# Kernel optimization log

Hardware: AMD Instinct MI355X
Metric: run time of the kernel (lower is better)

Reference implementation:

```python
import jax, jax.numpy as jnp
import numpy as np

HIDDEN = 2048
NUM_HEADS = 16
HEAD_DIM = HIDDEN // NUM_HEADS  # 128
ROPE_THETA = 10000.0
T = 4096


def _rope(x, positions):
    # x: [T, H, D]; neox-style rotary (rotate halves), matching vLLM get_rope default
    half = HEAD_DIM // 2
    inv_freq = 1.0 / (ROPE_THETA ** (jnp.arange(0, half, dtype=jnp.float32) / half))
    freqs = positions.astype(jnp.float32)[:, None] * inv_freq[None, :]  # [T, half]
    cos = jnp.cos(freqs)[:, None, :]  # [T, 1, half]
    sin = jnp.sin(freqs)[:, None, :]
    x1, x2 = x[..., :half], x[..., half:]
    return jnp.concatenate([x1 * cos - x2 * sin, x2 * cos + x1 * sin], axis=-1)


def setup_inputs() -> dict:
    key = jax.random.key(0)
    k1, k2, k3 = jax.random.split(key, 3)
    return {
        "hidden_states": jax.random.normal(k1, (T, HIDDEN), dtype=jnp.float32),
        "positions": jnp.arange(T, dtype=jnp.int32),
        "w_qkv": jax.random.normal(k2, (HIDDEN, 3 * HIDDEN), dtype=jnp.float32) * (HIDDEN ** -0.5),
        "w_o": jax.random.normal(k3, (HIDDEN, HIDDEN), dtype=jnp.float32) * (HIDDEN ** -0.5),
    }


def reference(hidden_states, positions, w_qkv, w_o):
    qkv = hidden_states @ w_qkv  # [T, 3H]
    q, k, v = jnp.split(qkv, 3, axis=-1)
    q = q.reshape(T, NUM_HEADS, HEAD_DIM)
    k = k.reshape(T, NUM_HEADS, HEAD_DIM)
    v = v.reshape(T, NUM_HEADS, HEAD_DIM)
    q = _rope(q, positions)
    k = _rope(k, positions)
    scale = HEAD_DIM ** -0.5
    # causal SDPA over flattened single sequence
    scores = jnp.einsum("qhd,khd->hqk", q, k) * scale  # [H, T, T]
    causal = jnp.tril(jnp.ones((T, T), dtype=bool))
    scores = jnp.where(causal[None, :, :], scores, jnp.finfo(scores.dtype).min)
    probs = jax.nn.softmax(scores, axis=-1)
    attn = jnp.einsum("hqk,khd->qhd", probs, v).reshape(T, HIDDEN)
    return attn @ w_o
```

## Files before the change

kernel.cpp:

```cpp
#include <hip/hip_runtime.h>
#include <hip/hip_bf16.h>
#include <cstdint>
#include <cstddef>

#define T_SEQ 4096
#define HID   2048
#define NH    16
#define HD    128
#define QKVN  6144
#define KVB   32
#define CHT   16
#define CPH   144

typedef unsigned short u16;
typedef unsigned int u32;
typedef __bf16 bf16x8 __attribute__((ext_vector_type(8)));
typedef __bf16 bf16x4 __attribute__((ext_vector_type(4)));
typedef float  f32x4  __attribute__((ext_vector_type(4)));

typedef const __attribute__((address_space(1))) void* gas_ptr;
typedef __attribute__((address_space(3))) void* las_ptr;

__device__ __forceinline__ void async16(const void* g, void* l) {
  __builtin_amdgcn_global_load_lds((gas_ptr)g, (las_ptr)l, 16, 0, 0);
}

__device__ __forceinline__ u16 f2bf(float f) {
  unsigned int u = __float_as_uint(f);
  u += 0x7fffu + ((u >> 16) & 1u);
  return (u16)(u >> 16);
}

__device__ __forceinline__ float bf2f(u16 x) {
  return __uint_as_float((unsigned)x << 16);
}

__global__ void cast_f32_bf16(const float* __restrict__ in, u16* __restrict__ out, int n) {
  int i = (blockIdx.x * blockDim.x + threadIdx.x) * 4;
  if (i >= n) return;
  float4 v = *(const float4*)&in[i];
  uint2 o;
  o.x = (unsigned)f2bf(v.x) | ((unsigned)f2bf(v.y) << 16);
  o.y = (unsigned)f2bf(v.z) | ((unsigned)f2bf(v.w) << 16);
  *(uint2*)&out[i] = o;
}

__global__ void transpose_cast(const float* __restrict__ in, u16* __restrict__ out,
                               int R, int C) {
  __shared__ float tile[64][65];
  int c0 = blockIdx.x * 64, r0 = blockIdx.y * 64;
  int tid = threadIdx.x;
#pragma unroll
  for (int i = 0; i < 16; ++i) {
    int e = i * 256 + tid;
    int rr = e >> 6, cc = e & 63;
    tile[rr][cc] = in[(size_t)(r0 + rr) * C + c0 + cc];
  }
  __syncthreads();
#pragma unroll
  for (int i = 0; i < 16; ++i) {
    int e = i * 256 + tid;
    int oc = e >> 6, orr = e & 63;
    out[(size_t)(c0 + oc) * R + r0 + orr] = f2bf(tile[orr][oc]);
  }
}

template <typename OUT>
__global__ __launch_bounds__(256)
void gemm_bf16_bt(const u16* __restrict__ A, const u16* __restrict__ BT,
                  OUT* __restrict__ C, int M, int N, int K) {
  __shared__ u16 As[2][128 * 32];
  __shared__ u16 Bs[2][128 * 32];
  int tid = threadIdx.x;
  int row0 = blockIdx.y * 128, col0 = blockIdx.x * 128;
  int wv = tid >> 6, lane = tid & 63, lr = lane & 15, lq = lane >> 4;
  int wm = (wv >> 1) * 64, wn = (wv & 1) * 64;
  f32x4 acc[4][4] = {};

  auto stage = [&](int buf, int ks) {
#pragma unroll
    for (int k = 0; k < 2; ++k) {
      int c = k * 256 + tid;
      int row = c >> 2, col = c & 3;
      int key = (row >> 1) & 3;
      async16(&A[(size_t)(row0 + row) * K + ks + (col ^ key) * 8], &As[buf][c * 8]);
      async16(&BT[(size_t)(col0 + row) * K + ks + (col ^ key) * 8], &Bs[buf][c * 8]);
    }
  };

  stage(0, 0);
  __syncthreads();
  int nk = K >> 5;
  for (int t = 0; t < nk; ++t) {
    int cur = t & 1;
    if (t + 1 < nk) stage(cur ^ 1, (t + 1) * 32);

    const char* AsB = (const char*)&As[cur][0];
    const char* BsB = (const char*)&Bs[cur][0];
    bf16x8 a[4], b[4];
#pragma unroll
    for (int mi = 0; mi < 4; ++mi) {
      int row = wm + mi * 16 + lr;
      a[mi] = *(const bf16x8*)(AsB + row * 64 + ((lq ^ ((row >> 1) & 3)) << 4));
    }
#pragma unroll
    for (int ni = 0; ni < 4; ++ni) {
      int row = wn + ni * 16 + lr;
      b[ni] = *(const bf16x8*)(BsB + row * 64 + ((lq ^ ((row >> 1) & 3)) << 4));
    }
#pragma unroll
    for (int mi = 0; mi < 4; ++mi)
#pragma unroll
      for (int ni = 0; ni < 4; ++ni)
        acc[mi][ni] = __builtin_amdgcn_mfma_f32_16x16x32_bf16(a[mi], b[ni], acc[mi][ni], 0, 0, 0);
    __syncthreads();
  }

#pragma unroll
  for (int mi = 0; mi < 4; ++mi)
#pragma unroll
    for (int ni = 0; ni < 4; ++ni)
#pragma unroll
      for (int r = 0; r < 4; ++r) {
        float v = acc[mi][ni][r];
        size_t idx = (size_t)(row0 + wm + mi * 16 + lq * 4 + r) * N + col0 + wn + ni * 16 + lr;
        if constexpr (sizeof(OUT) == 2) C[idx] = (OUT)f2bf(v);
        else                            C[idx] = (OUT)v;
      }
}

#define SCL2 0.12753224f

__global__ void rope_reorg(const u16* __restrict__ qkv, const int* __restrict__ pos,
                           u16* __restrict__ Qh, u16* __restrict__ Kh) {
  int idx = blockIdx.x * 256 + threadIdx.x;
  if (idx >= T_SEQ * NH * 64) return;
  int d = idx & 63;
  int h = (idx >> 6) & (NH - 1);
  int t = idx >> 10;
  float p = (float)pos[t];
  float inv = exp2f((float)d * -0.20762050594046932f);
  float f = p * inv;
  float s, c;
  __sincosf(f, &s, &c);

  size_t ib = (size_t)t * QKVN + h * HD + d;
  float q1 = bf2f(qkv[ib]), q2 = bf2f(qkv[ib + 64]);
  float k1 = bf2f(qkv[ib + HID]), k2 = bf2f(qkv[ib + HID + 64]);
  size_t ob = ((size_t)h * T_SEQ + t) * HD + d;
  Qh[ob]      = f2bf((q1 * c - q2 * s) * SCL2);
  Qh[ob + 64] = f2bf((q2 * c + q1 * s) * SCL2);
  Kh[ob]      = f2bf(k1 * c - k2 * s);
  Kh[ob + 64] = f2bf(k2 * c + k1 * s);
}

__global__ void vtrans(const u16* __restrict__ qkv, u16* __restrict__ Vt) {
  __shared__ u16 tile[64][136];
  int t0 = blockIdx.x * 64;
  int h = blockIdx.y;
  int tid = threadIdx.x;
#pragma unroll
  for (int i = 0; i < 32; ++i) {
    int e = i * 256 + tid;
    int tt = e >> 7, d = e & 127;
    tile[tt][d] = qkv[(size_t)(t0 + tt) * QKVN + 2 * HID + h * HD + d];
  }
  __syncthreads();
#pragma unroll
  for (int i = 0; i < 32; ++i) {
    int e = i * 256 + tid;
    int d = e >> 6, tt = e & 63;
    Vt[((size_t)h * HD + d) * T_SEQ + t0 + tt] = tile[tt][d];
  }
}

__global__ __launch_bounds__(256)
void attn_fwd(const u16* __restrict__ Qh, const u16* __restrict__ Kh,
              const u16* __restrict__ Vt, u16* __restrict__ Opart,
              float2* __restrict__ ml) {
  __shared__ u16 Ks[2][32 * 128];
  __shared__ u16 Vs[2][128 * 32];
  __shared__ u16 Ps[4][32 * 32];

  int tid = threadIdx.x;
  int wv = tid >> 6, lane = tid & 63, lr = lane & 15, lq = lane >> 4;
  char* PsB = (char*)&Ps[wv][0];

  int id = blockIdx.x;
  int h = id / CPH;
  int w = id - h * CPH;
  int bq = 0, acc = 0;
  for (;;) {
    int ch = (bq + 4) >> 2;
    if (w < acc + ch) break;
    acc += ch;
    ++bq;
  }
  int c = w - acc;
  int nt = 4 * bq + 4;
  int j0 = c * CHT, j1 = min(j0 + CHT, nt);
  int q0 = bq * 128, wrow0 = q0 + wv * 32;

  bf16x8 qf[2][4];
#pragma unroll
  for (int qi = 0; qi < 2; ++qi)
#pragma unroll
    for (int kd = 0; kd < 4; ++kd)
      qf[qi][kd] = *(const bf16x8*)
          &Qh[((size_t)h * T_SEQ + wrow0 + qi * 16 + lr) * HD + kd * 32 + lq * 8];

  f32x4 acc_ot[8][2] = {};
  float m_run[2] = {-1e30f, -1e30f};
  float l_run[2] = {0.0f, 0.0f};

  auto stage = [&](int buf, int jb) {
#pragma unroll
    for (int k = 0; k < 2; ++k) {
      int cc = k * 256 + tid;
      int row = cc >> 4;
      int sc = (cc ^ (row & 7)) & 15;
      async16(&Kh[((size_t)h * T_SEQ + jb + row) * HD + sc * 8], &Ks[buf][cc * 8]);
    }
#pragma unroll
    for (int k = 0; k < 2; ++k) {
      int cc = k * 256 + tid;
      int row = cc >> 2, col = cc & 3;
      int key = (row >> 1) & 3;
      async16(&Vt[((size_t)h * HD + row) * T_SEQ + jb + (col ^ key) * 8],
              &Vs[buf][cc * 8]);
    }
  };

  stage(0, j0 * KVB);
  __syncthreads();

  for (int j = j0; j < j1; ++j) {
    int cur = (j - j0) & 1;
    int jb = j * KVB;
    if (j + 1 < j1) stage(cur ^ 1, jb + KVB);

    if (jb <= wrow0 + 31) {
      const char* KsB = (const char*)&Ks[cur][0];
      const char* VsB = (const char*)&Vs[cur][0];

      f32x4 st[2][2] = {};
#pragma unroll
      for (int kd = 0; kd < 4; ++kd) {
#pragma unroll
        for (int kj = 0; kj < 2; ++kj) {
          int row = kj * 16 + lr;
          int byt = (row << 8) + kd * 64 + lq * 16;
          bf16x8 kf = *(const bf16x8*)(KsB + (byt ^ ((row & 7) << 4)));
#pragma unroll
          for (int qi = 0; qi < 2; ++qi)
            st[kj][qi] = __builtin_amdgcn_mfma_f32_16x16x32_bf16(
                kf, qf[qi][kd], st[kj][qi], 0, 0, 0);
        }
      }

      if (jb + KVB - 1 > wrow0) {
#pragma unroll
        for (int qi = 0; qi < 2; ++qi) {
          int qg = wrow0 + qi * 16 + lr;
#pragma unroll
          for (int kj = 0; kj < 2; ++kj)
#pragma unroll
            for (int r = 0; r < 4; ++r)
              if (jb + kj * 16 + lq * 4 + r > qg) st[kj][qi][r] = -1e30f;
        }
      }

      float sf[2];
#pragma unroll
      for (int qi = 0; qi < 2; ++qi) {
        float mx = fmaxf(fmaxf(fmaxf(st[0][qi][0], st[0][qi][1]),
                               fmaxf(st[0][qi][2], st[0][qi][3])),
                         fmaxf(fmaxf(st[1][qi][0], st[1][qi][1]),
                               fmaxf(st[1][qi][2], st[1][qi][3])));
        mx = fmaxf(mx, __shfl_xor(mx, 16));
        mx = fmaxf(mx, __shfl_xor(mx, 32));
        float mnew = fmaxf(m_run[qi], mx);
        sf[qi] = exp2f(m_run[qi] - mnew);
        m_run[qi] = mnew;

        int rowb = (qi * 16 + lr) * 64;
        int key = ((lr >> 1) & 3) << 4;
        float rs = 0.0f;
#pragma unroll
        for (int kj = 0; kj < 2; ++kj) {
          float p0 = exp2f(st[kj][qi][0] - mnew);
          float p1 = exp2f(st[kj][qi][1] - mnew);
          float p2 = exp2f(st[kj][qi][2] - mnew);
          float p3 = exp2f(st[kj][qi][3] - mnew);
          rs += (p0 + p1) + (p2 + p3);
          bf16x4 pk;
          pk[0] = (__bf16)p0; pk[1] = (__bf16)p1;
          pk[2] = (__bf16)p2; pk[3] = (__bf16)p3;
          *(bf16x4*)(PsB + rowb + (((kj * 16 + lq * 4) * 2) ^ key)) = pk;
        }
        l_run[qi] = l_run[qi] * sf[qi] + rs;
      }

      if (__any((sf[0] < 1.0f) || (sf[1] < 1.0f))) {
#pragma unroll
        for (int di = 0; di < 8; ++di)
#pragma unroll
          for (int qi = 0; qi < 2; ++qi)
#pragma unroll
            for (int r = 0; r < 4; ++r) acc_ot[di][qi][r] *= sf[qi];
      }

      bf16x8 pa[2];
#pragma unroll
      for (int qi = 0; qi < 2; ++qi) {
        int prow = qi * 16 + lr;
        pa[qi] = *(const bf16x8*)(PsB + prow * 64 + ((lq ^ ((lr >> 1) & 3)) << 4));
      }
#pragma unroll
      for (int di = 0; di < 8; ++di) {
        int vrow = di * 16 + lr;
        bf16x8 vb = *(const bf16x8*)(VsB + vrow * 64 + ((lq ^ ((vrow >> 1) & 3)) << 4));
#pragma unroll
        for (int qi = 0; qi < 2; ++qi)
          acc_ot[di][qi] = __builtin_amdgcn_mfma_f32_16x16x32_bf16(
              vb, pa[qi], acc_ot[di][qi], 0, 0, 0);
      }
    }
    __syncthreads();
  }

  u16* Op = Opart + (size_t)id * 128 * 128;
#pragma unroll
  for (int qi = 0; qi < 2; ++qi) {
    float l = l_run[qi];
    l += __shfl_xor(l, 16);
    l += __shfl_xor(l, 32);
    int q = wv * 32 + qi * 16 + lr;
    if (lq == 0) ml[(size_t)id * 128 + q] = make_float2(m_run[qi], l);
#pragma unroll
    for (int di = 0; di < 8; ++di) {
      bf16x4 pk;
      pk[0] = (__bf16)acc_ot[di][qi][0];
      pk[1] = (__bf16)acc_ot[di][qi][1];
      pk[2] = (__bf16)acc_ot[di][qi][2];
      pk[3] = (__bf16)acc_ot[di][qi][3];
      *(bf16x4*)&Op[q * 128 + di * 16 + lq * 4] = pk;
    }
  }
}

__global__ __launch_bounds__(256)
void attn_combine(const u16* __restrict__ Opart, const float2* __restrict__ ml,
                  u16* __restrict__ attn) {
  int idx = blockIdx.x * 256 + threadIdx.x;
  int e8 = idx * 8;
  int qrow = e8 >> 11;
  int col = e8 & (HID - 1);
  int h = col >> 7, coll = col & 127;
  int bq = qrow >> 7, ql = qrow & 127;
  int a = bq >> 2, r = bq & 3;
  int base = h * CPH + (a + 1) * (2 * a + r);
  int n = (bq + 4) >> 2;

  float m = -1e30f;
  for (int c = 0; c < n; ++c) m = fmaxf(m, ml[(size_t)(base + c) * 128 + ql].x);
  float lsum = 0.0f;
  float o[8] = {};
  for (int c = 0; c < n; ++c) {
    float2 mlc = ml[(size_t)(base + c) * 128 + ql];
    float wgt = exp2f(mlc.x - m);
    lsum += mlc.y * wgt;
    const u16* src = Opart + ((size_t)(base + c) * 128 + ql) * 128 + coll;
    ushort4 v0 = *(const ushort4*)src;
    ushort4 v1 = *(const ushort4*)(src + 4);
    o[0] += bf2f(v0.x) * wgt; o[1] += bf2f(v0.y) * wgt;
    o[2] += bf2f(v0.z) * wgt; o[3] += bf2f(v0.w) * wgt;
    o[4] += bf2f(v1.x) * wgt; o[5] += bf2f(v1.y) * wgt;
    o[6] += bf2f(v1.z) * wgt; o[7] += bf2f(v1.w) * wgt;
  }
  float rl = 1.0f / lsum;
  uint4 w;
  w.x = (u32)f2bf(o[0] * rl) | ((u32)f2bf(o[1] * rl) << 16);
  w.y = (u32)f2bf(o[2] * rl) | ((u32)f2bf(o[3] * rl) << 16);
  w.z = (u32)f2bf(o[4] * rl) | ((u32)f2bf(o[5] * rl) << 16);
  w.w = (u32)f2bf(o[6] * rl) | ((u32)f2bf(o[7] * rl) << 16);
  *(uint4*)&attn[e8] = w;
}

extern "C" void kernel_launch(void* const* d_in, const int* in_sizes, int n_in,
                              void* d_out, int out_size, void* d_ws, size_t ws_size,
                              hipStream_t stream) {
  const float* hidden    = (const float*)d_in[0];
  const int*   positions = (const int*)d_in[1];
  const float* w_qkv     = (const float*)d_in[2];
  const float* w_o       = (const float*)d_in[3];
  float* out = (float*)d_out;

  char* p = (char*)d_ws;
  u16* woT    = (u16*)p;  p += (size_t)HID * HID * 2;
  u16* Qh     = (u16*)p;  p += (size_t)T_SEQ * HID * 2;
  u16* Kh     = (u16*)p;  p += (size_t)T_SEQ * HID * 2;
  u16* Vt     = (u16*)p;  p += (size_t)T_SEQ * HID * 2;
  u16* attn_b = (u16*)p;  p += (size_t)T_SEQ * HID * 2;
  char* un = p;
  u16* hs_b   = (u16*)un;
  u16* wqkvT  = (u16*)(un + (size_t)T_SEQ * HID * 2);
  u16* qkvb   = (u16*)(un + (size_t)T_SEQ * HID * 2 + (size_t)QKVN * HID * 2);
  u16* Opart  = (u16*)un;
  float2* ml  = (float2*)(un + (size_t)NH * CPH * 128 * 128 * 2);

  cast_f32_bf16<<<(T_SEQ * HID / 4 + 255) / 256, 256, 0, stream>>>(hidden, hs_b, T_SEQ * HID);
  transpose_cast<<<dim3(QKVN / 64, HID / 64), 256, 0, stream>>>(w_qkv, wqkvT, HID, QKVN);
  transpose_cast<<<dim3(HID / 64, HID / 64), 256, 0, stream>>>(w_o, woT, HID, HID);
  gemm_bf16_bt<u16><<<dim3(QKVN / 128, T_SEQ / 128), 256, 0, stream>>>(hs_b, wqkvT, qkvb,
                                                                       T_SEQ, QKVN, HID);
  rope_reorg<<<(T_SEQ * NH * 64 + 255) / 256, 256, 0, stream>>>(qkvb, positions, Qh, Kh);
  vtrans<<<dim3(T_SEQ / 64, NH), 256, 0, stream>>>(qkvb, Vt);
  attn_fwd<<<NH * CPH, 256, 0, stream>>>(Qh, Kh, Vt, Opart, ml);
  attn_combine<<<T_SEQ * HID / 8 / 256, 256, 0, stream>>>(Opart, ml, attn_b);
  gemm_bf16_bt<float><<<dim3(HID / 128, T_SEQ / 128), 256, 0, stream>>>(attn_b, woT, out,
                                                                        T_SEQ, HID, HID);
}
```

Baseline: 419.6 us.

## Fuse RoPE and head reorg into QKV GEMM epilogue with precomputed cos/sin

Removes the separate rope_reorg kernel by applying rotary embedding and the Q scale directly in the QKV GEMM epilogue, writing Q and K straight into head-major layout. The warp tiling changes from 2x2 to 4x1, so each wave holds all 128 columns of a head and has both rotary halves in registers. A small cs_init kernel precomputes cos/sin per position. This avoids writing and re-reading Q/K through qkvb, at the cost of a wider B-fragment load per wave and strided stores in the epilogue.

```diff
diff --git a/kernel.cpp b/kernel.cpp
--- a/kernel.cpp
+++ b/kernel.cpp
@@ -11,6 +11,7 @@
 #define KVB   32
 #define CHT   16
 #define CPH   144
+#define SCL2  0.12753224f
 
 typedef unsigned short u16;
 typedef unsigned int u32;
@@ -65,17 +66,28 @@
   }
 }
 
-template <typename OUT>
+__global__ void cs_init(const int* __restrict__ pos, float2* __restrict__ cs) {
+  int idx = blockIdx.x * 256 + threadIdx.x;
+  int t = idx >> 6, dt = idx & 63;
+  float inv = exp2f((float)dt * -0.20762050594046932f);
+  float f = (float)pos[t] * inv;
+  float s, c;
+  __sincosf(f, &s, &c);
+  cs[idx] = make_float2(c, s);
+}
+
+template <int MODE, typename OUT>
 __global__ __launch_bounds__(256)
 void gemm_bf16_bt(const u16* __restrict__ A, const u16* __restrict__ BT,
-                  OUT* __restrict__ C, int M, int N, int K) {
+                  OUT* __restrict__ C, u16* __restrict__ Qh, u16* __restrict__ Kh,
+                  const float2* __restrict__ cs, int M, int N, int K) {
   __shared__ u16 As[2][128 * 32];
   __shared__ u16 Bs[2][128 * 32];
   int tid = threadIdx.x;
   int row0 = blockIdx.y * 128, col0 = blockIdx.x * 128;
   int wv = tid >> 6, lane = tid & 63, lr = lane & 15, lq = lane >> 4;
-  int wm = (wv >> 1) * 64, wn = (wv & 1) * 64;
-  f32x4 acc[4][4] = {};
+  int wm = wv * 32;
+  f32x4 acc[2][8] = {};
 
   auto stage = [&](int buf, int ks) {
 #pragma unroll
@@ -97,61 +109,67 @@
 
     const char* AsB = (const char*)&As[cur][0];
     const char* BsB = (const char*)&Bs[cur][0];
-    bf16x8 a[4], b[4];
-#pragma unroll
-    for (int mi = 0; mi < 4; ++mi) {
+    bf16x8 a[2], b[8];
+#pragma unroll
+    for (int mi = 0; mi < 2; ++mi) {
       int row = wm + mi * 16 + lr;
       a[mi] = *(const bf16x8*)(AsB + row * 64 + ((lq ^ ((row >> 1) & 3)) << 4));
     }
 #pragma unroll
-    for (int ni = 0; ni < 4; ++ni) {
-      int row = wn + ni * 16 + lr;
+    for (int ni = 0; ni < 8; ++ni) {
+      int row = ni * 16 + lr;
       b[ni] = *(const bf16x8*)(BsB + row * 64 + ((lq ^ ((row >> 1) & 3)) << 4));
     }
 #pragma unroll
-    for (int mi = 0; mi < 4; ++mi)
-#pragma unroll
-      for (int ni = 0; ni < 4; ++ni)
+    for (int mi = 0; mi < 2; ++mi)
+#pragma unroll
+      for (int ni = 0; ni < 8; ++ni)
         acc[mi][ni] = __builtin_amdgcn_mfma_f32_16x16x32_bf16(a[mi], b[ni], acc[mi][ni], 0, 0, 0);
     __syncthreads();
   }
 
-#pragma unroll
-  for (int mi = 0; mi < 4; ++mi)
-#pragma unroll
-    for (int ni = 0; ni < 4; ++ni)
-#pragma unroll
-      for (int r = 0; r < 4; ++r) {
-        float v = acc[mi][ni][r];
-        size_t idx = (size_t)(row0 + wm + mi * 16 + lq * 4 + r) * N + col0 + wn + ni * 16 + lr;
-        if constexpr (sizeof(OUT) == 2) C[idx] = (OUT)f2bf(v);
-        else                            C[idx] = (OUT)v;
-      }
-}
-
-#define SCL2 0.12753224f
-
-__global__ void rope_reorg(const u16* __restrict__ qkv, const int* __restrict__ pos,
-                           u16* __restrict__ Qh, u16* __restrict__ Kh) {
-  int idx = blockIdx.x * 256 + threadIdx.x;
-  if (idx >= T_SEQ * NH * 64) return;
-  int d = idx & 63;
-  int h = (idx >> 6) & (NH - 1);
-  int t = idx >> 10;
-  float p = (float)pos[t];
-  float inv = exp2f((float)d * -0.20762050594046932f);
-  float f = p * inv;
-  float s, c;
-  __sincosf(f, &s, &c);
-
-  size_t ib = (size_t)t * QKVN + h * HD + d;
-  float q1 = bf2f(qkv[ib]), q2 = bf2f(qkv[ib + 64]);
-  float k1 = bf2f(qkv[ib + HID]), k2 = bf2f(qkv[ib + HID + 64]);
-  size_t ob = ((size_t)h * T_SEQ + t) * HD + d;
-  Qh[ob]      = f2bf((q1 * c - q2 * s) * SCL2);
-  Qh[ob + 64] = f2bf((q2 * c + q1 * s) * SCL2);
-  Kh[ob]      = f2bf(k1 * c - k2 * s);
-  Kh[ob + 64] = f2bf(k2 * c + k1 * s);
+  if constexpr (MODE == 1) {
+    int sec = col0 >> 11;
+    int hh = (col0 & (HID - 1)) >> 7;
+    if (sec < 2) {
+      u16* dst = (sec == 0) ? Qh : Kh;
+      float scl = (sec == 0) ? SCL2 : 1.0f;
+#pragma unroll
+      for (int mi = 0; mi < 2; ++mi)
+#pragma unroll
+        for (int r = 0; r < 4; ++r) {
+          int t = row0 + wm + mi * 16 + lq * 4 + r;
+#pragma unroll
+          for (int nj = 0; nj < 4; ++nj) {
+            float2 csv = cs[t * 64 + nj * 16 + lr];
+            float v1 = acc[mi][nj][r], v2 = acc[mi][nj + 4][r];
+            float o1 = (v1 * csv.x - v2 * csv.y) * scl;
+            float o2 = (v2 * csv.x + v1 * csv.y) * scl;
+            size_t ob = ((size_t)hh * T_SEQ + t) * HD + nj * 16 + lr;
+            dst[ob] = f2bf(o1);
+            dst[ob + 64] = f2bf(o2);
+          }
+        }
+    } else {
+#pragma unroll
+      for (int mi = 0; mi < 2; ++mi)
+#pragma unroll
+        for (int ni = 0; ni < 8; ++ni)
+#pragma unroll
+          for (int r = 0; r < 4; ++r)
+            C[(size_t)(row0 + wm + mi * 16 + lq * 4 + r) * N + col0 + ni * 16 + lr] =
+                (OUT)f2bf(acc[mi][ni][r]);
+    }
+  } else {
+#pragma unroll
+    for (int mi = 0; mi < 2; ++mi)
+#pragma unroll
+      for (int ni = 0; ni < 8; ++ni)
+#pragma unroll
+        for (int r = 0; r < 4; ++r)
+          C[(size_t)(row0 + wm + mi * 16 + lq * 4 + r) * N + col0 + ni * 16 + lr] =
+              (OUT)acc[mi][ni][r];
+  }
 }
 
 __global__ void vtrans(const u16* __restrict__ qkv, u16* __restrict__ Vt) {
@@ -402,6 +420,7 @@
   u16* Kh     = (u16*)p;  p += (size_t)T_SEQ * HID * 2;
   u16* Vt     = (u16*)p;  p += (size_t)T_SEQ * HID * 2;
   u16* attn_b = (u16*)p;  p += (size_t)T_SEQ * HID * 2;
+  float2* cs  = (float2*)p; p += (size_t)T_SEQ * 64 * sizeof(float2);
   char* un = p;
   u16* hs_b   = (u16*)un;
   u16* wqkvT  = (u16*)(un + (size_t)T_SEQ * HID * 2);
@@ -412,12 +431,12 @@
   cast_f32_bf16<<<(T_SEQ * HID / 4 + 255) / 256, 256, 0, stream>>>(hidden, hs_b, T_SEQ * HID);
   transpose_cast<<<dim3(QKVN / 64, HID / 64), 256, 0, stream>>>(w_qkv, wqkvT, HID, QKVN);
   transpose_cast<<<dim3(HID / 64, HID / 64), 256, 0, stream>>>(w_o, woT, HID, HID);
-  gemm_bf16_bt<u16><<<dim3(QKVN / 128, T_SEQ / 128), 256, 0, stream>>>(hs_b, wqkvT, qkvb,
-                                                                       T_SEQ, QKVN, HID);
-  rope_reorg<<<(T_SEQ * NH * 64 + 255) / 256, 256, 0, stream>>>(qkvb, positions, Qh, Kh);
+  cs_init<<<T_SEQ * 64 / 256, 256, 0, stream>>>(positions, cs);
+  gemm_bf16_bt<1, u16><<<dim3(QKVN / 128, T_SEQ / 128), 256, 0, stream>>>(
+      hs_b, wqkvT, qkvb, Qh, Kh, cs, T_SEQ, QKVN, HID);
   vtrans<<<dim3(T_SEQ / 64, NH), 256, 0, stream>>>(qkvb, Vt);
   attn_fwd<<<NH * CPH, 256, 0, stream>>>(Qh, Kh, Vt, Opart, ml);
   attn_combine<<<T_SEQ * HID / 8 / 256, 256, 0, stream>>>(Opart, ml, attn_b);
-  gemm_bf16_bt<float><<<dim3(HID / 128, T_SEQ / 128), 256, 0, stream>>>(attn_b, woT, out,
-                                                                        T_SEQ, HID, HID);
-}
+  gemm_bf16_bt<0, float><<<dim3(HID / 128, T_SEQ / 128), 256, 0, stream>>>(
+      attn_b, woT, out, nullptr, nullptr, nullptr, T_SEQ, HID, HID);
+}
```

New measurement: 406.3 us. 3.2% less time.
